# Performance work log

Measured on AMD Instinct MI355X. Metric: run time of the kernel, lower is better.

Reference implementation:

```python
import jax, jax.numpy as jnp
import numpy as np
import itertools

CONVEX_K = 10
NUM_CLASS = 100
B, N = 8, 16384
MINDIS_INIT = 1.0e5  # torch code initializes mindis to 100000


def _hull_vertex_labels_np(pts):
    """pts: [G, K, 3] numpy. Exact brute-force 3D convex hull vertex labels
    (general position): a triple is a hull facet iff all points lie on one
    side of its plane; every point on some facet is a hull vertex."""
    G, K, _ = pts.shape
    tri = np.array(list(itertools.combinations(range(K), 3)))  # [T,3]
    a = pts[:, tri[:, 0]]                                      # [G,T,3]
    b = pts[:, tri[:, 1]]
    c = pts[:, tri[:, 2]]
    n = np.cross(b - a, c - a)                                 # [G,T,3]
    d = np.einsum('gkd,gtd->gtk', pts, n) - np.einsum('gtd,gtd->gt', a, n)[:, :, None]
    eps = 1e-7
    facet = (d <= eps).all(-1) | (d >= -eps).all(-1)           # [G,T]
    labels = np.zeros((G, K), dtype=np.int32)
    gidx, tidx = np.nonzero(facet)
    for col in range(3):
        labels[gidx, tri[tidx, col]] = 1
    return labels


def setup_inputs() -> dict:
    key = jax.random.key(0)
    k1, k2, k3 = jax.random.split(key, 3)
    xyz = jax.random.normal(k1, (B, N, 6), dtype=jnp.float32)
    skel_xyz = jax.random.normal(k2, (B, NUM_CLASS * CONVEX_K, 3), dtype=jnp.float32)
    weights = jax.random.normal(k3, (B, NUM_CLASS * CONVEX_K // CONVEX_K * CONVEX_K,), dtype=jnp.float32)[:, :NUM_CLASS * CONVEX_K].reshape(B, -1)[:, :1000]
    weights = jax.random.normal(k3, (B, NUM_CLASS * CONVEX_K), dtype=jnp.float32)
    skel_np = np.asarray(skel_xyz).reshape(B * NUM_CLASS, CONVEX_K, 3)
    labels = jnp.asarray(_hull_vertex_labels_np(skel_np).reshape(B, NUM_CLASS, CONVEX_K))
    return {"xyz": xyz, "skel_xyz": skel_xyz, "weights": weights,
            "labels": labels, "num_class": NUM_CLASS}


def reference(xyz, skel_xyz, weights, labels, num_class):
    b = xyz.shape[0]
    pts = xyz[:, :, :3]                                   # [B,N,3]; normals xyz[:,:,3:6] unused
    cp = skel_xyz.reshape(b, num_class, CONVEX_K, 3)      # [B,C,K,3]

    # --- convex loss: for each non-vertex point, min sq-dist to a hull vertex ---
    diff = cp[:, :, :, None, :] - cp[:, :, None, :, :]    # [B,C,K,K,3] (small)
    sqd = jnp.sum(diff * diff, axis=-1)                   # [B,C,K,K]
    is_vert = labels == 1                                  # [B,C,K]
    masked = jnp.where(is_vert[:, :, None, :], sqd, jnp.inf)
    mindis = jnp.minimum(jnp.min(masked, axis=-1), MINDIS_INIT)  # [B,C,K]
    loss_convex = jnp.sum(jnp.where(is_vert, 0.0, mindis)) / (b * num_class)

    # --- Chamfer (closest_distance_with_batch both directions, L2 norm, summed) ---
    skel = skel_xyz                                        # [B,M,3]
    d2 = (jnp.sum(pts * pts, -1)[:, :, None]
          + jnp.sum(skel * skel, -1)[:, None, :]
          - 2.0 * jnp.einsum('bnd,bmd->bnm', pts, skel))   # [B,N,M]
    d = jnp.sqrt(jnp.maximum(d2, 1e-12))
    loss_cd = (jnp.sum(jnp.min(d, axis=2)) + jnp.sum(jnp.min(d, axis=1))) / b

    return 1.0 * loss_convex + 0.1 * loss_cd
```

## Files before the change

### kernel.cpp

```cpp
#include <hip/hip_runtime.h>

#define BATCH 8
#define NPTS 16384
#define MSKEL 1000
#define NCLS 100
#define CKK 10
#define MINDIS_INITF 100000.0f

#define OFF_PTSM 32000
#define OFF_MINB (32000 + 524288)

__global__ __launch_bounds__(256) void k_prep(const float* __restrict__ xyz,
                                              const float* __restrict__ skel,
                                              float4* __restrict__ skelN,
                                              float4* __restrict__ ptsM,
                                              unsigned int* __restrict__ minbits,
                                              float* __restrict__ out) {
    const int gid = blockIdx.x * 256 + threadIdx.x;
    {
        const float* p = xyz + (size_t)gid * 6;
        float x = p[0], y = p[1], z = p[2];
        ptsM[gid] = make_float4(x, y, z, 0.5f * (x * x + y * y + z * z));
    }
    if (gid < BATCH * MSKEL) {
        const float* s = skel + (size_t)gid * 3;
        float sx = s[0], sy = s[1], sz = s[2];
        skelN[gid] = make_float4(-sx, -sy, -sz, 0.5f * (sx * sx + sy * sy + sz * sz));
        minbits[gid] = 0x7F800000u;
    }
    if (gid == 0) out[0] = 0.0f;
}

__global__ __launch_bounds__(256) void k_chamfer(const float4* __restrict__ skelN,
                                                 const float4* __restrict__ ptsM,
                                                 unsigned int* __restrict__ minbits,
                                                 float* __restrict__ out) {
    const int bid = blockIdx.x;
    const int tid = threadIdx.x;

    if (bid < 256) {
        const int b = bid >> 5, tile = bid & 31;
        const int wave = tid >> 6, lane = tid & 63;
        const float4* __restrict__ base = ptsM + b * NPTS + tile * 512;

        float4 P[8];
        float mt[8];
#pragma unroll
        for (int j = 0; j < 8; ++j) {
            P[j] = base[j * 64 + lane];
            mt[j] = 3.4e38f;
        }

        const float4* __restrict__ sk = skelN + b * MSKEL + wave * 250;
#pragma unroll 5
        for (int m = 0; m < 250; ++m) {
            float4 s = sk[m];
#pragma unroll
            for (int j = 0; j < 8; ++j) {
                float t = fmaf(P[j].x, s.x, fmaf(P[j].y, s.y, fmaf(P[j].z, s.z, s.w)));
                mt[j] = fminf(mt[j], t);
            }
        }

        __shared__ float sm[4 * 512];
#pragma unroll
        for (int j = 0; j < 8; ++j) {
            sm[wave * 512 + j * 64 + lane] = mt[j] + P[j].w;
        }
        __syncthreads();

        float a0 = fminf(fminf(sm[tid], sm[512 + tid]),
                         fminf(sm[1024 + tid], sm[1536 + tid]));
        float a1 = fminf(fminf(sm[tid + 256], sm[512 + tid + 256]),
                         fminf(sm[1024 + tid + 256], sm[1536 + tid + 256]));
        float d = sqrtf(fmaxf(2.0f * a0, 1e-12f)) + sqrtf(fmaxf(2.0f * a1, 1e-12f));

#pragma unroll
        for (int o = 32; o > 0; o >>= 1) d += __shfl_down(d, o, 64);
        __shared__ float s_part[4];
        if (lane == 0) s_part[wave] = d;
        __syncthreads();
        if (tid == 0) {
            atomicAdd(out, 0.0125f * (s_part[0] + s_part[1] + s_part[2] + s_part[3]));
        }
    } else {
        const int id = bid - 256;
        const int b = id >> 5, tile = id & 31;

        float nsx[4], nsy[4], nsz[4], ssq[4], mind[4];
#pragma unroll
        for (int k = 0; k < 4; ++k) {
            const int m = tid + k * 256;
            if (m < MSKEL) {
                float4 s = skelN[b * MSKEL + m];
                nsx[k] = s.x; nsy[k] = s.y; nsz[k] = s.z;
                ssq[k] = 2.0f * s.w;
            } else {
                nsx[k] = 0.0f; nsy[k] = 0.0f; nsz[k] = 0.0f; ssq[k] = 0.0f;
            }
            mind[k] = 3.4e38f;
        }

        const float4* __restrict__ pp = ptsM + b * NPTS + tile * 512;
#pragma unroll 8
        for (int n = 0; n < 512; ++n) {
            float4 r = pp[n];
#pragma unroll
            for (int k = 0; k < 4; ++k) {
                float t = fmaf(r.x, nsx[k], fmaf(r.y, nsy[k], fmaf(r.z, nsz[k], r.w)));
                mind[k] = fminf(mind[k], t);
            }
        }
#pragma unroll
        for (int k = 0; k < 4; ++k) {
            const int m = tid + k * 256;
            if (m < MSKEL) {
                float d2 = fmaf(2.0f, mind[k], ssq[k]);
                atomicMin(&minbits[b * MSKEL + m], __float_as_uint(fmaxf(d2, 0.0f)));
            }
        }
    }
}

__global__ __launch_bounds__(256) void k_reduce(const float* __restrict__ skel,
                                                const int* __restrict__ labels,
                                                const unsigned int* __restrict__ minbits,
                                                float* __restrict__ out) {
    const int gid = blockIdx.x * 256 + threadIdx.x;
    const int tid = threadIdx.x;
    float acc = 0.0f;

    for (int i = gid; i < BATCH * MSKEL; i += 2048) {
        acc += 0.0125f * sqrtf(fmaxf(__uint_as_float(minbits[i]), 1e-12f));
    }

    if (gid < BATCH * NCLS) {
        const int b = gid / NCLS, c = gid - b * NCLS;
        const float* cp = skel + ((size_t)b * MSKEL + c * CKK) * 3;
        const int* lab = labels + (size_t)b * NCLS * CKK + c * CKK;
        float x[CKK], y[CKK], z[CKK];
        int lv[CKK];
#pragma unroll
        for (int i = 0; i < CKK; ++i) {
            x[i] = cp[i * 3 + 0]; y[i] = cp[i * 3 + 1]; z[i] = cp[i * 3 + 2];
            lv[i] = lab[i];
        }
        float convexSum = 0.0f;
#pragma unroll
        for (int i = 0; i < CKK; ++i) {
            if (lv[i] != 1) {
                float mind = MINDIS_INITF;
#pragma unroll
                for (int j = 0; j < CKK; ++j) {
                    if (lv[j] == 1) {
                        float dx = x[i] - x[j], dy = y[i] - y[j], dz = z[i] - z[j];
                        mind = fminf(mind, dx * dx + dy * dy + dz * dz);
                    }
                }
                convexSum += mind;
            }
        }
        acc += convexSum * (1.0f / (BATCH * NCLS));
    }

#pragma unroll
    for (int o = 32; o > 0; o >>= 1) acc += __shfl_down(acc, o, 64);
    __shared__ float s_part[4];
    const int wave = tid >> 6, lane = tid & 63;
    if (lane == 0) s_part[wave] = acc;
    __syncthreads();
    if (tid == 0) {
        atomicAdd(out, s_part[0] + s_part[1] + s_part[2] + s_part[3]);
    }
}

extern "C" void kernel_launch(void* const* d_in, const int* in_sizes, int n_in,
                              void* d_out, int out_size, void* d_ws, size_t ws_size,
                              hipStream_t stream) {
    const float* xyz = (const float*)d_in[0];
    const float* skel = (const float*)d_in[1];
    const int* labels = (const int*)d_in[3];
    float* out = (float*)d_out;

    float4* skelN = (float4*)d_ws;
    float4* ptsM = (float4*)((float*)d_ws + OFF_PTSM);
    unsigned int* minbits = (unsigned int*)((float*)d_ws + OFF_MINB);

    k_prep<<<512, 256, 0, stream>>>(xyz, skel, skelN, ptsM, minbits, out);
    k_chamfer<<<512, 256, 0, stream>>>(skelN, ptsM, minbits, out);
    k_reduce<<<8, 256, 0, stream>>>(skel, labels, minbits, out);
}
```

Baseline: 93.10 us.

## Enlarge chamfer register tiles and use 512-thread blocks

The point-to-skeleton half now keeps 16 points per lane and splits the skeleton across 8 waves, so each loaded skeleton entry feeds twice as many FMAs. The skeleton-to-point half gives each thread 8 consecutive skeleton entries and splits the points into 4 groups of 256, which also raises the FMA count per broadcast point load. The launch changes to 256 blocks of 512 threads. With 256 large blocks on a GPU with many CUs, occupancy and load balance may drop, and the higher register count may cap the number of waves that can run at once.

```diff
diff --git a/kernel.cpp b/kernel.cpp
--- a/kernel.cpp
+++ b/kernel.cpp
@@ -31,91 +31,95 @@
     if (gid == 0) out[0] = 0.0f;
 }
 
-__global__ __launch_bounds__(256) void k_chamfer(const float4* __restrict__ skelN,
-                                                 const float4* __restrict__ ptsM,
-                                                 unsigned int* __restrict__ minbits,
-                                                 float* __restrict__ out) {
+__global__ __launch_bounds__(512, 2) void k_chamfer(const float4* __restrict__ skelN,
+                                                    const float4* __restrict__ ptsM,
+                                                    unsigned int* __restrict__ minbits,
+                                                    float* __restrict__ out) {
     const int bid = blockIdx.x;
     const int tid = threadIdx.x;
+    const int wave = tid >> 6, lane = tid & 63;
 
-    if (bid < 256) {
-        const int b = bid >> 5, tile = bid & 31;
-        const int wave = tid >> 6, lane = tid & 63;
-        const float4* __restrict__ base = ptsM + b * NPTS + tile * 512;
+    if (bid < 128) {
+        const int b = bid >> 4, tile = bid & 15;
+        const float4* __restrict__ base = ptsM + b * NPTS + tile * 1024;
 
-        float4 P[8];
-        float mt[8];
+        float4 P[16];
+        float mt[16];
 #pragma unroll
-        for (int j = 0; j < 8; ++j) {
+        for (int j = 0; j < 16; ++j) {
             P[j] = base[j * 64 + lane];
             mt[j] = 3.4e38f;
         }
 
-        const float4* __restrict__ sk = skelN + b * MSKEL + wave * 250;
+        const float4* __restrict__ sk = skelN + b * MSKEL + wave * 125;
 #pragma unroll 5
-        for (int m = 0; m < 250; ++m) {
+        for (int m = 0; m < 125; ++m) {
             float4 s = sk[m];
 #pragma unroll
-            for (int j = 0; j < 8; ++j) {
+            for (int j = 0; j < 16; ++j) {
                 float t = fmaf(P[j].x, s.x, fmaf(P[j].y, s.y, fmaf(P[j].z, s.z, s.w)));
                 mt[j] = fminf(mt[j], t);
             }
         }
 
-        __shared__ float sm[4 * 512];
+        __shared__ float sm[8 * 1024];
 #pragma unroll
-        for (int j = 0; j < 8; ++j) {
-            sm[wave * 512 + j * 64 + lane] = mt[j] + P[j].w;
+        for (int j = 0; j < 16; ++j) {
+            sm[wave * 1024 + j * 64 + lane] = mt[j] + P[j].w;
         }
         __syncthreads();
 
-        float a0 = fminf(fminf(sm[tid], sm[512 + tid]),
-                         fminf(sm[1024 + tid], sm[1536 + tid]));
-        float a1 = fminf(fminf(sm[tid + 256], sm[512 + tid + 256]),
-                         fminf(sm[1024 + tid + 256], sm[1536 + tid + 256]));
+        float a0 = sm[tid], a1 = sm[tid + 512];
+#pragma unroll
+        for (int w = 1; w < 8; ++w) {
+            a0 = fminf(a0, sm[w * 1024 + tid]);
+            a1 = fminf(a1, sm[w * 1024 + tid + 512]);
+        }
         float d = sqrtf(fmaxf(2.0f * a0, 1e-12f)) + sqrtf(fmaxf(2.0f * a1, 1e-12f));
 
 #pragma unroll
         for (int o = 32; o > 0; o >>= 1) d += __shfl_down(d, o, 64);
-        __shared__ float s_part[4];
+        __shared__ float s_part[8];
         if (lane == 0) s_part[wave] = d;
         __syncthreads();
         if (tid == 0) {
-            atomicAdd(out, 0.0125f * (s_part[0] + s_part[1] + s_part[2] + s_part[3]));
+            float sum = 0.0f;
+#pragma unroll
+            for (int w = 0; w < 8; ++w) sum += s_part[w];
+            atomicAdd(out, 0.0125f * sum);
         }
     } else {
-        const int id = bid - 256;
-        const int b = id >> 5, tile = id & 31;
+        const int id = bid - 128;
+        const int b = id >> 4, tile = id & 15;
+        const int group = tid >> 7;
+        const int local = tid & 127;
+        const int m0 = local * 8;
 
-        float nsx[4], nsy[4], nsz[4], ssq[4], mind[4];
+        float4 S[8];
+        float mind[8];
 #pragma unroll
-        for (int k = 0; k < 4; ++k) {
-            const int m = tid + k * 256;
-            if (m < MSKEL) {
-                float4 s = skelN[b * MSKEL + m];
-                nsx[k] = s.x; nsy[k] = s.y; nsz[k] = s.z;
-                ssq[k] = 2.0f * s.w;
-            } else {
-                nsx[k] = 0.0f; nsy[k] = 0.0f; nsz[k] = 0.0f; ssq[k] = 0.0f;
-            }
+        for (int k = 0; k < 8; ++k) {
+            const int m = m0 + k;
+            S[k] = (m < MSKEL) ? skelN[b * MSKEL + m]
+                               : make_float4(0.0f, 0.0f, 0.0f, 0.0f);
             mind[k] = 3.4e38f;
         }
 
-        const float4* __restrict__ pp = ptsM + b * NPTS + tile * 512;
+        const float4* __restrict__ pp = ptsM + b * NPTS + tile * 1024 + group * 256;
 #pragma unroll 8
-        for (int n = 0; n < 512; ++n) {
+        for (int n = 0; n < 256; ++n) {
             float4 r = pp[n];
 #pragma unroll
-            for (int k = 0; k < 4; ++k) {
-                float t = fmaf(r.x, nsx[k], fmaf(r.y, nsy[k], fmaf(r.z, nsz[k], r.w)));
+            for (int k = 0; k < 8; ++k) {
+                float t = fmaf(r.x, S[k].x, fmaf(r.y, S[k].y, fmaf(r.z, S[k].z, r.w)));
                 mind[k] = fminf(mind[k], t);
             }
         }
 #pragma unroll
-        for (int k = 0; k < 4; ++k) {
-            const int m = tid + k * 256;
+        for (int k = 0; k < 8; ++k) {
+            const int m = m0 + k;
             if (m < MSKEL) {
-                float d2 = fmaf(2.0f, mind[k], ssq[k]);
+                float d2 = 2.0f * (mind[k] + S[k].w);
                 atomicMin(&minbits[b * MSKEL + m], __float_as_uint(fmaxf(d2, 0.0f)));
             }
         }
@@ -187,6 +191,6 @@
     unsigned int* minbits = (unsigned int*)((float*)d_ws + OFF_MINB);
 
     k_prep<<<512, 256, 0, stream>>>(xyz, skel, skelN, ptsM, minbits, out);
-    k_chamfer<<<512, 256, 0, stream>>>(skelN, ptsM, minbits, out);
+    k_chamfer<<<256, 512, 0, stream>>>(skelN, ptsM, minbits, out);
     k_reduce<<<8, 256, 0, stream>>>(skel, labels, minbits, out);
 }
```

Result: slower. 107.4 us (+15.4%).
